# Optimization experiments

Hardware: AMD Instinct MI355X
Metric: run time of the kernel (lower is better)

The kernel has to match this reference:

```python
import jax, jax.numpy as jnp
import numpy as np

N_NODES = 100000
N_EDGES = 1600000
IN_DIM = 128
HIDDEN = 128
OUT_DIM = 64


def setup_inputs() -> dict:
    key = jax.random.key(0)
    k_x, k_e, k_w1, k_b1, k_w2, k_b2 = jax.random.split(key, 6)
    x = jax.random.normal(k_x, (N_NODES, IN_DIM), dtype=jnp.float32)
    edge_index = jax.random.randint(k_e, (2, N_EDGES), 0, N_NODES, dtype=jnp.int64)
    # GCNConv weight/bias (glorot-ish scale) and final Linear head
    W1 = jax.random.normal(k_w1, (IN_DIM, HIDDEN), dtype=jnp.float32) / np.sqrt(IN_DIM)
    b1 = jnp.zeros((HIDDEN,), dtype=jnp.float32)
    W2 = jax.random.normal(k_w2, (HIDDEN, OUT_DIM), dtype=jnp.float32) / np.sqrt(HIDDEN)
    b2 = jnp.zeros((OUT_DIM,), dtype=jnp.float32)
    return {"x": x, "W1": W1, "b1": b1, "W2": W2, "b2": b2, "edge_index": edge_index}


def _gcn_conv(x, W, b, src, dst, norm, n_nodes):
    # PyG GCNConv: linear transform, then sym-normalized neighbor aggregation
    h = x @ W                                   # (N, H) dense transform
    msg = h[src] * norm[:, None]                # (E+N, H) gather + scale
    out = jax.ops.segment_sum(msg, dst, num_segments=n_nodes)  # scatter-add
    return out + b


def reference(x, W1, b1, W2, b2, edge_index):
    n = x.shape[0]
    # add self-loops (PyG GCNConv default)
    loop = jnp.arange(n, dtype=edge_index.dtype)
    src = jnp.concatenate([edge_index[0], loop])
    dst = jnp.concatenate([edge_index[1], loop])
    # symmetric normalization D^{-1/2} A D^{-1/2}
    deg = jnp.zeros((n,), dtype=x.dtype).at[dst].add(1.0)
    dinv = jnp.where(deg > 0, jax.lax.rsqrt(jnp.maximum(deg, 1.0)), 0.0)
    norm = dinv[src] * dinv[dst]

    h = _gcn_conv(x, W1, b1, src, dst, norm, n)
    h = jax.nn.relu(h)
    # dropout: identity in eval/inference mode
    return h @ W2 + b2
```

## Files before the change

kernel.cpp:

```cpp
#include <hip/hip_runtime.h>

#define N_NODES 100000
#define N_EDGES 1600000
#define IN_DIM  128
#define HIDDEN  128
#define OUT_DIM 64

#define BUCK_SHIFT 6
#define BUCK_SZ    64
#define NB_BUCK ((N_NODES + BUCK_SZ - 1) / BUCK_SZ)
#define EPB 4096
#define NBLK_E ((N_EDGES + EPB - 1) / EPB)
#define GB1 ((N_NODES + 127) / 128)
#define CAP 1536
#define PCAP 1984

typedef __attribute__((ext_vector_type(8))) short bf8_t;
typedef __attribute__((ext_vector_type(4))) float f4_t;

__device__ __forceinline__ ushort f2b(float f) {
    unsigned int u = __float_as_uint(f);
    u += 0x7fffu + ((u >> 16) & 1u);
    return (ushort)(u >> 16);
}
__device__ __forceinline__ float b2f_lo(unsigned int u) { return __uint_as_float(u << 16); }
__device__ __forceinline__ float b2f_hi(unsigned int u) { return __uint_as_float(u & 0xffff0000u); }


__global__ __launch_bounds__(256, 2) void k_fuse1(const int* __restrict__ ei,
                                                  int* __restrict__ cursor,
                                                  unsigned int* __restrict__ part,
                                                  const float* __restrict__ x,
                                                  const float* __restrict__ W1,
                                                  ushort* __restrict__ h) {
    __shared__ __align__(16) ushort smem[2 * 128 * 136];
    int tid = threadIdx.x;

    if (blockIdx.x < NBLK_E) {
        int* lh    = (int*)smem;
        int* lbase = lh + NB_BUCK;
        for (int i = tid; i < NB_BUCK; i += 256) lh[i] = 0;
        __syncthreads();
        int e0 = blockIdx.x * EPB;
        int srcv[EPB / 256], dstv[EPB / 256];
        #pragma unroll
        for (int j = 0; j < EPB / 256; j++) {
            int e = e0 + j * 256 + tid;
            if (e < N_EDGES) {
                srcv[j] = ei[e];
                dstv[j] = ei[N_EDGES + e];
                atomicAdd(&lh[dstv[j] >> BUCK_SHIFT], 1);
            } else dstv[j] = -1;
        }
        __syncthreads();
        for (int i = tid; i < NB_BUCK; i += 256) {
            int c = lh[i];
            lbase[i] = (c > 0) ? (i * CAP + atomicAdd(&cursor[i], c)) : 0;
            lh[i] = 0;
        }
        __syncthreads();
        #pragma unroll
        for (int j = 0; j < EPB / 256; j++) {
            if (dstv[j] >= 0) {
                int b = dstv[j] >> BUCK_SHIFT;
                int pos = lbase[b] + atomicAdd(&lh[b], 1);
                part[pos] = ((unsigned int)(dstv[j] & (BUCK_SZ - 1)) << 24) | (unsigned int)srcv[j];
            }
        }
        return;
    }

    typedef ushort (*tile_t)[136];
    tile_t As = (tile_t)smem;
    tile_t Bs = (tile_t)(smem + 128 * 136);
    int row0 = (blockIdx.x - NBLK_E) * 128;
    const int M = N_NODES;

    #pragma unroll
    for (int i = 0; i < 16; i++) {
        int li = tid + i * 256;
        int r = li >> 5, c4 = li & 31;
        int grow = row0 + r; if (grow > M - 1) grow = M - 1;
        float4 v = *(const float4*)(x + (size_t)grow * 128 + c4 * 4);
        ushort4 o;
        o.x = f2b(v.x); o.y = f2b(v.y); o.z = f2b(v.z); o.w = f2b(v.w);
        *(ushort4*)&As[r][c4 * 4] = o;
    }
    #pragma unroll
    for (int i = 0; i < 16; i++) {
        int li = tid + i * 256;
        int k = li >> 5, n4 = li & 31;
        float4 v = *(const float4*)(W1 + (size_t)k * 128 + n4 * 4);
        Bs[n4 * 4 + 0][k] = f2b(v.x);
        Bs[n4 * 4 + 1][k] = f2b(v.y);
        Bs[n4 * 4 + 2][k] = f2b(v.z);
        Bs[n4 * 4 + 3][k] = f2b(v.w);
    }
    __syncthreads();

    int wave = tid >> 6, lane = tid & 63;
    int lr = lane & 15, lq = lane >> 4;
    int wm0 = (wave & 1) * 64;
    int wn0 = (wave >> 1) * 64;

    f4_t acc[4][4];
    #pragma unroll
    for (int mi = 0; mi < 4; mi++)
        #pragma unroll
        for (int ni = 0; ni < 4; ni++) acc[mi][ni] = (f4_t){0.f, 0.f, 0.f, 0.f};

    #pragma unroll
    for (int kb = 0; kb < 4; kb++) {
        bf8_t af[4], bfr[4];
        #pragma unroll
        for (int mi = 0; mi < 4; mi++)
            af[mi] = *(const bf8_t*)&As[wm0 + mi * 16 + lr][kb * 32 + lq * 8];
        #pragma unroll
        for (int ni = 0; ni < 4; ni++)
            bfr[ni] = *(const bf8_t*)&Bs[wn0 + ni * 16 + lr][kb * 32 + lq * 8];
        #pragma unroll
        for (int mi = 0; mi < 4; mi++)
            #pragma unroll
            for (int ni = 0; ni < 4; ni++)
                acc[mi][ni] = __builtin_amdgcn_mfma_f32_16x16x32_bf16(
                    af[mi], bfr[ni], acc[mi][ni], 0, 0, 0);
    }

    #pragma unroll
    for (int mi = 0; mi < 4; mi++) {
        #pragma unroll
        for (int r = 0; r < 4; r++) {
            int row = row0 + wm0 + mi * 16 + lq * 4 + r;
            if (row < M) {
                #pragma unroll
                for (int ni = 0; ni < 4; ni++)
                    h[(size_t)row * 128 + wn0 + ni * 16 + lr] = f2b(acc[mi][ni][r]);
            }
        }
    }
}


__global__ __launch_bounds__(256) void k_csr(const unsigned int* __restrict__ part,
                                             const int* __restrict__ cursor,
                                             int* __restrict__ offs,
                                             int* __restrict__ pcnt,
                                             float* __restrict__ dinv,
                                             int* __restrict__ ssrc,
                                             ushort* __restrict__ h) {
    __shared__ int ldeg[BUCK_SZ], lsc[BUCK_SZ], lcur[BUCK_SZ], sob[BUCK_SZ];
    __shared__ unsigned int stage[CAP];
    int t = threadIdx.x;
    int b = blockIdx.x;
    int rbeg = b * CAP;
    int cnt = cursor[b];
    int node0 = b << BUCK_SHIFT;
    if (b == 0) {
        if (t == 0) dinv[N_NODES] = 0.f;
        if (t < 128) h[(size_t)N_NODES * 128 + t] = 0;
    }
    if (t < BUCK_SZ) ldeg[t] = 0;
    __syncthreads();
    for (int i = t; i < cnt; i += 256) {
        unsigned int u = part[rbeg + i];
        stage[i] = u;
        atomicAdd(&ldeg[u >> 24], 1);
    }
    __syncthreads();
    int v = 0, pv = 0;
    if (t < BUCK_SZ) {
        v = ldeg[t];
        pv = (v + 7) & ~7;
        lsc[t] = pv;
    }
    __syncthreads();
    for (int off = 1; off < BUCK_SZ; off <<= 1) {
        int add = 0;
        if (t < BUCK_SZ && t >= off) add = lsc[t - off];
        __syncthreads();
        if (t < BUCK_SZ) lsc[t] += add;
        __syncthreads();
    }
    if (t < BUCK_SZ) {
        int ob = b * PCAP + (lsc[t] - pv);
        sob[t] = ob;
        lcur[t] = 0;
        if (node0 + t < N_NODES) {
            offs[node0 + t] = ob;
            pcnt[node0 + t] = pv;
            dinv[node0 + t] = rsqrtf((float)(v + 1));
        }
    }
    __syncthreads();
    for (int i = t; i < cnt; i += 256) {
        unsigned int u = stage[i];
        int d = u >> 24;
        int pos = atomicAdd(&lcur[d], 1);
        ssrc[sob[d] + pos] = (int)(u & 0xFFFFFFu);
    }
    if (t < BUCK_SZ)
        for (int i = v; i < pv; i++) ssrc[sob[t] + i] = N_NODES;
}


__global__ __launch_bounds__(256, 7) void k_agg2(const ushort* __restrict__ h,
                                                 const int* __restrict__ offs,
                                                 const int* __restrict__ pcnt,
                                                 const int* __restrict__ ssrc,
                                                 const float* __restrict__ dinv,
                                                 const float* __restrict__ b1,
                                                 const float* __restrict__ W2,
                                                 const float* __restrict__ b2,
                                                 float* __restrict__ out) {
    __shared__ ushort As[16][136];
    __shared__ ushort Bs[64][136];
    int tid = threadIdx.x;
    int wave = tid >> 6, lane = tid & 63;
    int base = blockIdx.x * 16;

    #pragma unroll
    for (int i = 0; i < 8; i++) {
        int li = tid + i * 256;
        int k = li >> 4, n4 = li & 15;
        float4 v = *(const float4*)(W2 + (size_t)k * 64 + n4 * 4);
        Bs[n4 * 4 + 0][k] = f2b(v.x);
        Bs[n4 * 4 + 1][k] = f2b(v.y);
        Bs[n4 * 4 + 2][k] = f2b(v.z);
        Bs[n4 * 4 + 3][k] = f2b(v.w);
    }

    const unsigned int* hp = (const unsigned int*)h;
    float2 bb = ((const float2*)b1)[lane];

    #pragma unroll 1
    for (int j = 0; j < 4; j++) {
        int r = wave * 4 + j;
        int n = base + r;
        int e0 = __builtin_amdgcn_readfirstlane(offs[n]);
        int iters = __builtin_amdgcn_readfirstlane(pcnt[n]) >> 3;
        const uint4* ip = (const uint4*)(ssrc + e0);

        float ax0 = 0.f, ay0 = 0.f, ax1 = 0.f, ay1 = 0.f;
        float ax2 = 0.f, ay2 = 0.f, ax3 = 0.f, ay3 = 0.f;
        uint4 i0, i1;
        if (iters > 0) { i0 = ip[0]; i1 = ip[1]; }
        for (int it = 0; it < iters; it++) {
            uint4 nx0 = i0, nx1 = i1;
            if (it + 1 < iters) { nx0 = ip[(it + 1) * 2]; nx1 = ip[(it + 1) * 2 + 1]; }
            int s0 = __builtin_amdgcn_readfirstlane((int)i0.x);
            int s1 = __builtin_amdgcn_readfirstlane((int)i0.y);
            int s2 = __builtin_amdgcn_readfirstlane((int)i0.z);
            int s3 = __builtin_amdgcn_readfirstlane((int)i0.w);
            int s4 = __builtin_amdgcn_readfirstlane((int)i1.x);
            int s5 = __builtin_amdgcn_readfirstlane((int)i1.y);
            int s6 = __builtin_amdgcn_readfirstlane((int)i1.z);
            int s7 = __builtin_amdgcn_readfirstlane((int)i1.w);
            unsigned int u0 = (hp + ((unsigned)s0 << 6))[lane];
            unsigned int u1 = (hp + ((unsigned)s1 << 6))[lane];
            unsigned int u2 = (hp + ((unsigned)s2 << 6))[lane];
            unsigned int u3 = (hp + ((unsigned)s3 << 6))[lane];
            unsigned int u4 = (hp + ((unsigned)s4 << 6))[lane];
            unsigned int u5 = (hp + ((unsigned)s5 << 6))[lane];
            unsigned int u6 = (hp + ((unsigned)s6 << 6))[lane];
            unsigned int u7 = (hp + ((unsigned)s7 << 6))[lane];
            float w0 = dinv[s0], w1 = dinv[s1], w2 = dinv[s2], w3 = dinv[s3];
            float w4 = dinv[s4], w5 = dinv[s5], w6 = dinv[s6], w7 = dinv[s7];
            ax0 = fmaf(b2f_lo(u0), w0, ax0); ay0 = fmaf(b2f_hi(u0), w0, ay0);
            ax1 = fmaf(b2f_lo(u1), w1, ax1); ay1 = fmaf(b2f_hi(u1), w1, ay1);
            ax2 = fmaf(b2f_lo(u2), w2, ax2); ay2 = fmaf(b2f_hi(u2), w2, ay2);
            ax3 = fmaf(b2f_lo(u3), w3, ax3); ay3 = fmaf(b2f_hi(u3), w3, ay3);
            ax0 = fmaf(b2f_lo(u4), w4, ax0); ay0 = fmaf(b2f_hi(u4), w4, ay0);
            ax1 = fmaf(b2f_lo(u5), w5, ax1); ay1 = fmaf(b2f_hi(u5), w5, ay1);
            ax2 = fmaf(b2f_lo(u6), w6, ax2); ay2 = fmaf(b2f_hi(u6), w6, ay2);
            ax3 = fmaf(b2f_lo(u7), w7, ax3); ay3 = fmaf(b2f_hi(u7), w7, ay3);
            i0 = nx0; i1 = nx1;
        }
        unsigned int us = hp[(size_t)n * 64 + lane];
        float dn = dinv[n];
        float rx = (ax0 + ax1 + ax2 + ax3 + b2f_lo(us) * dn) * dn + bb.x;
        float ry = (ay0 + ay1 + ay2 + ay3 + b2f_hi(us) * dn) * dn + bb.y;
        rx = rx > 0.f ? rx : 0.f;
        ry = ry > 0.f ? ry : 0.f;
        *(unsigned int*)&As[r][lane * 2] =
            ((unsigned int)f2b(ry) << 16) | (unsigned int)f2b(rx);
    }
    __syncthreads();

    int lr = lane & 15, lq = lane >> 4;
    f4_t acc = (f4_t){0.f, 0.f, 0.f, 0.f};
    #pragma unroll
    for (int kb = 0; kb < 4; kb++) {
        bf8_t af = *(const bf8_t*)&As[lr][kb * 32 + lq * 8];
        bf8_t bf = *(const bf8_t*)&Bs[wave * 16 + lr][kb * 32 + lq * 8];
        acc = __builtin_amdgcn_mfma_f32_16x16x32_bf16(af, bf, acc, 0, 0, 0);
    }
    int col = wave * 16 + lr;
    float bv = b2[col];
    #pragma unroll
    for (int r = 0; r < 4; r++) {
        int node = base + lq * 4 + r;
        out[(size_t)node * 64 + col] = acc[r] + bv;
    }
}


extern "C" void kernel_launch(void* const* d_in, const int* in_sizes, int n_in,
                              void* d_out, int out_size, void* d_ws, size_t ws_size,
                              hipStream_t stream) {
    const float* x  = (const float*)d_in[0];
    const float* W1 = (const float*)d_in[1];
    const float* b1 = (const float*)d_in[2];
    const float* W2 = (const float*)d_in[3];
    const float* b2 = (const float*)d_in[4];
    const int*   ei = (const int*)d_in[5];
    float* out = (float*)d_out;

    char* w = (char*)d_ws;
    size_t off = 0;
    auto alloc = [&](size_t bytes) -> void* {
        void* p = w + off;
        off += (bytes + 255) & ~(size_t)255;
        return p;
    };
    ushort* h      = (ushort*)alloc((size_t)(N_NODES + 1) * HIDDEN * 2);
    float* dinv    = (float*)alloc((size_t)(N_NODES + 1) * 4);
    int*   offs    = (int*)alloc((size_t)N_NODES * 4);
    int*   pcnt    = (int*)alloc((size_t)N_NODES * 4);
    int*   ssrc    = (int*)alloc((size_t)NB_BUCK * PCAP * 4);
    unsigned int* part = (unsigned int*)alloc((size_t)NB_BUCK * CAP * 4);
    int*   cursor  = (int*)alloc((size_t)NB_BUCK * 4);

    hipMemsetAsync(cursor, 0, (size_t)NB_BUCK * 4, stream);
    k_fuse1<<<NBLK_E + GB1, 256, 0, stream>>>(ei, cursor, part, x, W1, h);
    k_csr<<<NB_BUCK, 256, 0, stream>>>(part, cursor, offs, pcnt, dinv, ssrc, h);
    k_agg2<<<N_NODES / 16, 256, 0, stream>>>(h, offs, pcnt, ssrc, dinv, b1, W2, b2, out);
}
```

Measured before the change: 217.5 us.

## Split edge bucketing into count, scan, and scatter kernels; pre-convert W1 once

Replaces the single-pass bucketing, which used global atomics on per-bucket cursors, with three kernels. The first counts edges per block and bucket, the second runs a per-bucket prefix scan over blocks, and the third writes edges deterministically using only shared-memory atomics. W1 is converted to bf16 in transposed layout once by a small prep kernel, and the GEMM blocks read it straight from global memory instead of each staging it in LDS. This halves LDS use so occupancy can rise. The cost is three extra launches, edge_index being read twice, and a serial scan of about 391 steps per bucket.

```diff
diff --git a/kernel.cpp b/kernel.cpp
--- a/kernel.cpp
+++ b/kernel.cpp
@@ -14,6 +14,7 @@
 #define GB1 ((N_NODES + 127) / 128)
 #define CAP 1536
 #define PCAP 1984
+#define CSTRIDE 1600
 
 typedef __attribute__((ext_vector_type(8))) short bf8_t;
 typedef __attribute__((ext_vector_type(4))) float f4_t;
@@ -26,53 +27,43 @@
 __device__ __forceinline__ float b2f_lo(unsigned int u) { return __uint_as_float(u << 16); }
 __device__ __forceinline__ float b2f_hi(unsigned int u) { return __uint_as_float(u & 0xffff0000u); }
 
-
-__global__ __launch_bounds__(256, 2) void k_fuse1(const int* __restrict__ ei,
-                                                  int* __restrict__ cursor,
-                                                  unsigned int* __restrict__ part,
-                                                  const float* __restrict__ x,
-                                                  const float* __restrict__ W1,
-                                                  ushort* __restrict__ h) {
-    __shared__ __align__(16) ushort smem[2 * 128 * 136];
+__global__ __launch_bounds__(256) void k_prep(const float* __restrict__ W1,
+                                              ushort* __restrict__ w1b) {
+    int start = blockIdx.x * 2048;
+    #pragma unroll
+    for (int j = 0; j < 8; j++) {
+        int i = start + j * 256 + threadIdx.x;
+        int n = i >> 7, k = i & 127;
+        w1b[i] = f2b(W1[k * 128 + n]);
+    }
+}
+
+__global__ __launch_bounds__(256, 3) void k_cnt(const int* __restrict__ ei,
+                                                int* __restrict__ counts,
+                                                const float* __restrict__ x,
+                                                const ushort* __restrict__ w1b,
+                                                ushort* __restrict__ h) {
+    __shared__ __align__(16) ushort smem[128 * 136];
     int tid = threadIdx.x;
 
     if (blockIdx.x < NBLK_E) {
-        int* lh    = (int*)smem;
-        int* lbase = lh + NB_BUCK;
+        int* lh = (int*)smem;
         for (int i = tid; i < NB_BUCK; i += 256) lh[i] = 0;
         __syncthreads();
         int e0 = blockIdx.x * EPB;
-        int srcv[EPB / 256], dstv[EPB / 256];
         #pragma unroll
         for (int j = 0; j < EPB / 256; j++) {
             int e = e0 + j * 256 + tid;
-            if (e < N_EDGES) {
-                srcv[j] = ei[e];
-                dstv[j] = ei[N_EDGES + e];
-                atomicAdd(&lh[dstv[j] >> BUCK_SHIFT], 1);
-            } else dstv[j] = -1;
+            if (e < N_EDGES) atomicAdd(&lh[ei[N_EDGES + e] >> BUCK_SHIFT], 1);
         }
         __syncthreads();
-        for (int i = tid; i < NB_BUCK; i += 256) {
-            int c = lh[i];
-            lbase[i] = (c > 0) ? (i * CAP + atomicAdd(&cursor[i], c)) : 0;
-            lh[i] = 0;
-        }
-        __syncthreads();
-        #pragma unroll
-        for (int j = 0; j < EPB / 256; j++) {
-            if (dstv[j] >= 0) {
-                int b = dstv[j] >> BUCK_SHIFT;
-                int pos = lbase[b] + atomicAdd(&lh[b], 1);
-                part[pos] = ((unsigned int)(dstv[j] & (BUCK_SZ - 1)) << 24) | (unsigned int)srcv[j];
-            }
-        }
+        for (int i = tid; i < NB_BUCK; i += 256)
+            counts[(size_t)blockIdx.x * CSTRIDE + i] = lh[i];
         return;
     }
 
     typedef ushort (*tile_t)[136];
     tile_t As = (tile_t)smem;
-    tile_t Bs = (tile_t)(smem + 128 * 136);
     int row0 = (blockIdx.x - NBLK_E) * 128;
     const int M = N_NODES;
 
@@ -86,16 +77,6 @@
         o.x = f2b(v.x); o.y = f2b(v.y); o.z = f2b(v.z); o.w = f2b(v.w);
         *(ushort4*)&As[r][c4 * 4] = o;
     }
-    #pragma unroll
-    for (int i = 0; i < 16; i++) {
-        int li = tid + i * 256;
-        int k = li >> 5, n4 = li & 31;
-        float4 v = *(const float4*)(W1 + (size_t)k * 128 + n4 * 4);
-        Bs[n4 * 4 + 0][k] = f2b(v.x);
-        Bs[n4 * 4 + 1][k] = f2b(v.y);
-        Bs[n4 * 4 + 2][k] = f2b(v.z);
-        Bs[n4 * 4 + 3][k] = f2b(v.w);
-    }
     __syncthreads();
 
     int wave = tid >> 6, lane = tid & 63;
@@ -117,7 +98,7 @@
             af[mi] = *(const bf8_t*)&As[wm0 + mi * 16 + lr][kb * 32 + lq * 8];
         #pragma unroll
         for (int ni = 0; ni < 4; ni++)
-            bfr[ni] = *(const bf8_t*)&Bs[wn0 + ni * 16 + lr][kb * 32 + lq * 8];
+            bfr[ni] = *(const bf8_t*)(w1b + (size_t)(wn0 + ni * 16 + lr) * 128 + kb * 32 + lq * 8);
         #pragma unroll
         for (int mi = 0; mi < 4; mi++)
             #pragma unroll
@@ -140,6 +121,41 @@
     }
 }
 
+__global__ __launch_bounds__(256) void k_scan(int* __restrict__ counts,
+                                              int* __restrict__ cursor) {
+    int b = blockIdx.x * 256 + threadIdx.x;
+    if (b >= NB_BUCK) return;
+    int run = b * CAP;
+    #pragma unroll 8
+    for (int blk = 0; blk < NBLK_E; blk++) {
+        size_t idx = (size_t)blk * CSTRIDE + b;
+        int c = counts[idx];
+        counts[idx] = run;
+        run += c;
+    }
+    cursor[b] = run - b * CAP;
+}
+
+__global__ __launch_bounds__(256, 8) void k_part(const int* __restrict__ ei,
+                                                 const int* __restrict__ counts,
+                                                 unsigned int* __restrict__ part) {
+    __shared__ int lcur[NB_BUCK];
+    int tid = threadIdx.x, blk = blockIdx.x;
+    for (int i = tid; i < NB_BUCK; i += 256)
+        lcur[i] = counts[(size_t)blk * CSTRIDE + i];
+    __syncthreads();
+    int e0 = blk * EPB;
+    #pragma unroll
+    for (int j = 0; j < EPB / 256; j++) {
+        int e = e0 + j * 256 + tid;
+        if (e < N_EDGES) {
+            int src = ei[e], dst = ei[N_EDGES + e];
+            int b = dst >> BUCK_SHIFT;
+            int pos = atomicAdd(&lcur[b], 1);
+            part[pos] = ((unsigned int)(dst & (BUCK_SZ - 1)) << 24) | (unsigned int)src;
+        }
+    }
+}
 
 __global__ __launch_bounds__(256) void k_csr(const unsigned int* __restrict__ part,
                                              const int* __restrict__ cursor,
@@ -201,7 +217,6 @@
     if (t < BUCK_SZ)
         for (int i = v; i < pv; i++) ssrc[sob[t] + i] = N_NODES;
 }
-
 
 __global__ __launch_bounds__(256, 7) void k_agg2(const ushort* __restrict__ h,
                                                  const int* __restrict__ offs,
@@ -329,9 +344,13 @@
     int*   ssrc    = (int*)alloc((size_t)NB_BUCK * PCAP * 4);
     unsigned int* part = (unsigned int*)alloc((size_t)NB_BUCK * CAP * 4);
     int*   cursor  = (int*)alloc((size_t)NB_BUCK * 4);
-
-    hipMemsetAsync(cursor, 0, (size_t)NB_BUCK * 4, stream);
-    k_fuse1<<<NBLK_E + GB1, 256, 0, stream>>>(ei, cursor, part, x, W1, h);
+    int*   counts  = (int*)alloc((size_t)NBLK_E * CSTRIDE * 4);
+    ushort* w1b    = (ushort*)alloc((size_t)HIDDEN * IN_DIM * 2);
+
+    k_prep<<<8, 256, 0, stream>>>(W1, w1b);
+    k_cnt<<<NBLK_E + GB1, 256, 0, stream>>>(ei, counts, x, w1b, h);
+    k_scan<<<(NB_BUCK + 255) / 256, 256, 0, stream>>>(counts, cursor);
+    k_part<<<NBLK_E, 256, 0, stream>>>(ei, counts, part);
     k_csr<<<NB_BUCK, 256, 0, stream>>>(part, cursor, offs, pcnt, dinv, ssrc, h);
     k_agg2<<<N_NODES / 16, 256, 0, stream>>>(h, offs, pcnt, ssrc, dinv, b1, W2, b2, out);
 }
```

Measured after the change: 262.1 us. 1.21x slower.

## Replace bucketed CSR build with per-node degree count and direct atomic scatter

Applied to the files above, without the earlier changes.

Replaces the two-pass bucket partition and staging kernel with a global per-node degree histogram, a wave-level scan kernel that computes padded offsets and dinv, and a scatter kernel that places each source directly using per-node atomic cursors. W1 is converted to transposed bf16 once in a small pre-kernel, and the GEMM reads it from global memory instead of building a shared B tile per block, halving shared memory. This removes the part buffer and the intermediate bucket pass. In exchange the edge list is read twice, global atomics on random node addresses are more contended and scattered, and there is one more kernel launch.

```diff
diff --git a/kernel.cpp b/kernel.cpp
--- a/kernel.cpp
+++ b/kernel.cpp
@@ -12,7 +12,6 @@
 #define EPB 4096
 #define NBLK_E ((N_EDGES + EPB - 1) / EPB)
 #define GB1 ((N_NODES + 127) / 128)
-#define CAP 1536
 #define PCAP 1984
 
 typedef __attribute__((ext_vector_type(8))) short bf8_t;
@@ -26,45 +25,83 @@
 __device__ __forceinline__ float b2f_lo(unsigned int u) { return __uint_as_float(u << 16); }
 __device__ __forceinline__ float b2f_hi(unsigned int u) { return __uint_as_float(u & 0xffff0000u); }
 
-
-__global__ __launch_bounds__(256, 2) void k_fuse1(const int* __restrict__ ei,
-                                                  int* __restrict__ cursor,
-                                                  unsigned int* __restrict__ part,
-                                                  const float* __restrict__ x,
-                                                  const float* __restrict__ W1,
-                                                  ushort* __restrict__ h) {
-    __shared__ __align__(16) ushort smem[2 * 128 * 136];
+__global__ __launch_bounds__(256) void k_cp(const int* __restrict__ ei,
+                                            int* __restrict__ deg,
+                                            const float* __restrict__ W1,
+                                            ushort* __restrict__ w1b,
+                                            float* __restrict__ dinv,
+                                            ushort* __restrict__ h) {
     int tid = threadIdx.x;
+    int b = blockIdx.x;
+    if (b < NBLK_E) {
+        int e0 = b * EPB;
+        #pragma unroll
+        for (int j = 0; j < EPB / 256; j++) {
+            int e = e0 + j * 256 + tid;
+            if (e < N_EDGES) atomicAdd(&deg[ei[N_EDGES + e]], 1);
+        }
+        return;
+    }
+    int start = (b - NBLK_E) * 2048;
+    #pragma unroll
+    for (int j = 0; j < 8; j++) {
+        int i = start + j * 256 + tid;
+        int n = i >> 7, k = i & 127;
+        w1b[i] = f2b(W1[k * 128 + n]);
+    }
+    if (b == NBLK_E) {
+        if (tid == 0) dinv[N_NODES] = 0.f;
+        if (tid < 128) h[(size_t)N_NODES * 128 + tid] = 0;
+    }
+}
+
+__global__ __launch_bounds__(256) void k_off(const int* __restrict__ deg,
+                                             int* __restrict__ offs,
+                                             int* __restrict__ pcnt,
+                                             int* __restrict__ ncur,
+                                             float* __restrict__ dinv,
+                                             int* __restrict__ ssrc) {
+    int wave = threadIdx.x >> 6, lane = threadIdx.x & 63;
+    int b = blockIdx.x * 4 + wave;
+    if (b >= NB_BUCK) return;
+    int n = (b << BUCK_SHIFT) + lane;
+    int v = (n < N_NODES) ? deg[n] : 0;
+    int pv = (v + 7) & ~7;
+    int sc = pv;
+    #pragma unroll
+    for (int off = 1; off < 64; off <<= 1) {
+        int u = __shfl_up(sc, off, 64);
+        if (lane >= off) sc += u;
+    }
+    int ob = b * PCAP + (sc - pv);
+    if (n < N_NODES) {
+        offs[n] = ob;
+        pcnt[n] = pv;
+        ncur[n] = 0;
+        dinv[n] = rsqrtf((float)(v + 1));
+        for (int i = v; i < pv; i++) ssrc[ob + i] = N_NODES;
+    }
+}
+
+__global__ __launch_bounds__(256, 3) void k_sg(const int* __restrict__ ei,
+                                               const int* __restrict__ offs,
+                                               int* __restrict__ ncur,
+                                               int* __restrict__ ssrc,
+                                               const float* __restrict__ x,
+                                               const ushort* __restrict__ w1b,
+                                               ushort* __restrict__ h) {
+    __shared__ __align__(16) ushort smem[128 * 136];
+    int tid = threadIdx.x;
 
     if (blockIdx.x < NBLK_E) {
-        int* lh    = (int*)smem;
-        int* lbase = lh + NB_BUCK;
-        for (int i = tid; i < NB_BUCK; i += 256) lh[i] = 0;
-        __syncthreads();
         int e0 = blockIdx.x * EPB;
-        int srcv[EPB / 256], dstv[EPB / 256];
         #pragma unroll
         for (int j = 0; j < EPB / 256; j++) {
             int e = e0 + j * 256 + tid;
             if (e < N_EDGES) {
-                srcv[j] = ei[e];
-                dstv[j] = ei[N_EDGES + e];
-                atomicAdd(&lh[dstv[j] >> BUCK_SHIFT], 1);
-            } else dstv[j] = -1;
-        }
-        __syncthreads();
-        for (int i = tid; i < NB_BUCK; i += 256) {
-            int c = lh[i];
-            lbase[i] = (c > 0) ? (i * CAP + atomicAdd(&cursor[i], c)) : 0;
-            lh[i] = 0;
-        }
-        __syncthreads();
-        #pragma unroll
-        for (int j = 0; j < EPB / 256; j++) {
-            if (dstv[j] >= 0) {
-                int b = dstv[j] >> BUCK_SHIFT;
-                int pos = lbase[b] + atomicAdd(&lh[b], 1);
-                part[pos] = ((unsigned int)(dstv[j] & (BUCK_SZ - 1)) << 24) | (unsigned int)srcv[j];
+                int src = ei[e], dst = ei[N_EDGES + e];
+                int pos = atomicAdd(&ncur[dst], 1);
+                ssrc[offs[dst] + pos] = src;
             }
         }
         return;
@@ -72,7 +109,6 @@
 
     typedef ushort (*tile_t)[136];
     tile_t As = (tile_t)smem;
-    tile_t Bs = (tile_t)(smem + 128 * 136);
     int row0 = (blockIdx.x - NBLK_E) * 128;
     const int M = N_NODES;
 
@@ -86,16 +122,6 @@
         o.x = f2b(v.x); o.y = f2b(v.y); o.z = f2b(v.z); o.w = f2b(v.w);
         *(ushort4*)&As[r][c4 * 4] = o;
     }
-    #pragma unroll
-    for (int i = 0; i < 16; i++) {
-        int li = tid + i * 256;
-        int k = li >> 5, n4 = li & 31;
-        float4 v = *(const float4*)(W1 + (size_t)k * 128 + n4 * 4);
-        Bs[n4 * 4 + 0][k] = f2b(v.x);
-        Bs[n4 * 4 + 1][k] = f2b(v.y);
-        Bs[n4 * 4 + 2][k] = f2b(v.z);
-        Bs[n4 * 4 + 3][k] = f2b(v.w);
-    }
     __syncthreads();
 
     int wave = tid >> 6, lane = tid & 63;
@@ -117,7 +143,7 @@
             af[mi] = *(const bf8_t*)&As[wm0 + mi * 16 + lr][kb * 32 + lq * 8];
         #pragma unroll
         for (int ni = 0; ni < 4; ni++)
-            bfr[ni] = *(const bf8_t*)&Bs[wn0 + ni * 16 + lr][kb * 32 + lq * 8];
+            bfr[ni] = *(const bf8_t*)(w1b + (size_t)(wn0 + ni * 16 + lr) * 128 + kb * 32 + lq * 8);
         #pragma unroll
         for (int mi = 0; mi < 4; mi++)
             #pragma unroll
@@ -139,69 +165,6 @@
         }
     }
 }
-
-
-__global__ __launch_bounds__(256) void k_csr(const unsigned int* __restrict__ part,
-                                             const int* __restrict__ cursor,
-                                             int* __restrict__ offs,
-                                             int* __restrict__ pcnt,
-                                             float* __restrict__ dinv,
-                                             int* __restrict__ ssrc,
-                                             ushort* __restrict__ h) {
-    __shared__ int ldeg[BUCK_SZ], lsc[BUCK_SZ], lcur[BUCK_SZ], sob[BUCK_SZ];
-    __shared__ unsigned int stage[CAP];
-    int t = threadIdx.x;
-    int b = blockIdx.x;
-    int rbeg = b * CAP;
-    int cnt = cursor[b];
-    int node0 = b << BUCK_SHIFT;
-    if (b == 0) {
-        if (t == 0) dinv[N_NODES] = 0.f;
-        if (t < 128) h[(size_t)N_NODES * 128 + t] = 0;
-    }
-    if (t < BUCK_SZ) ldeg[t] = 0;
-    __syncthreads();
-    for (int i = t; i < cnt; i += 256) {
-        unsigned int u = part[rbeg + i];
-        stage[i] = u;
-        atomicAdd(&ldeg[u >> 24], 1);
-    }
-    __syncthreads();
-    int v = 0, pv = 0;
-    if (t < BUCK_SZ) {
-        v = ldeg[t];
-        pv = (v + 7) & ~7;
-        lsc[t] = pv;
-    }
-    __syncthreads();
-    for (int off = 1; off < BUCK_SZ; off <<= 1) {
-        int add = 0;
-        if (t < BUCK_SZ && t >= off) add = lsc[t - off];
-        __syncthreads();
-        if (t < BUCK_SZ) lsc[t] += add;
-        __syncthreads();
-    }
-    if (t < BUCK_SZ) {
-        int ob = b * PCAP + (lsc[t] - pv);
-        sob[t] = ob;
-        lcur[t] = 0;
-        if (node0 + t < N_NODES) {
-            offs[node0 + t] = ob;
-            pcnt[node0 + t] = pv;
-            dinv[node0 + t] = rsqrtf((float)(v + 1));
-        }
-    }
-    __syncthreads();
-    for (int i = t; i < cnt; i += 256) {
-        unsigned int u = stage[i];
-        int d = u >> 24;
-        int pos = atomicAdd(&lcur[d], 1);
-        ssrc[sob[d] + pos] = (int)(u & 0xFFFFFFu);
-    }
-    if (t < BUCK_SZ)
-        for (int i = v; i < pv; i++) ssrc[sob[t] + i] = N_NODES;
-}
-
 
 __global__ __launch_bounds__(256, 7) void k_agg2(const ushort* __restrict__ h,
                                                  const int* __restrict__ offs,
@@ -326,12 +289,14 @@
     float* dinv    = (float*)alloc((size_t)(N_NODES + 1) * 4);
     int*   offs    = (int*)alloc((size_t)N_NODES * 4);
     int*   pcnt    = (int*)alloc((size_t)N_NODES * 4);
+    int*   ncur    = (int*)alloc((size_t)N_NODES * 4);
+    int*   deg     = (int*)alloc((size_t)N_NODES * 4);
     int*   ssrc    = (int*)alloc((size_t)NB_BUCK * PCAP * 4);
-    unsigned int* part = (unsigned int*)alloc((size_t)NB_BUCK * CAP * 4);
-    int*   cursor  = (int*)alloc((size_t)NB_BUCK * 4);
-
-    hipMemsetAsync(cursor, 0, (size_t)NB_BUCK * 4, stream);
-    k_fuse1<<<NBLK_E + GB1, 256, 0, stream>>>(ei, cursor, part, x, W1, h);
-    k_csr<<<NB_BUCK, 256, 0, stream>>>(part, cursor, offs, pcnt, dinv, ssrc, h);
+    ushort* w1b    = (ushort*)alloc((size_t)HIDDEN * IN_DIM * 2);
+
+    hipMemsetAsync(deg, 0, (size_t)N_NODES * 4, stream);
+    k_cp<<<NBLK_E + 8, 256, 0, stream>>>(ei, deg, W1, w1b, dinv, h);
+    k_off<<<(NB_BUCK + 3) / 4, 256, 0, stream>>>(deg, offs, pcnt, ncur, dinv, ssrc);
+    k_sg<<<NBLK_E + GB1, 256, 0, stream>>>(ei, offs, ncur, ssrc, x, w1b, h);
     k_agg2<<<N_NODES / 16, 256, 0, stream>>>(h, offs, pcnt, ssrc, dinv, b1, W2, b2, out);
 }
```

New measurement: 323.3 us. 1.49x slower.

## Pre-convert weights to bf16 once and read MFMA B operands from global

Applied to the files above, without the earlier changes.

Adds a small prep kernel that transposes W1 and W2 to bf16 once. The GEMM and aggregation kernels then load their B fragments straight from global or L2 instead of re-staging the weights into shared memory in every block. This halves shared memory in k_fuse1 and removes Bs from k_agg2, and the occupancy hints are raised to match. Edge binning now uses 16384 edges per block and re-reads the edge indices in the second pass instead of holding them in registers. The cost is one extra launch, repeated global loads of the B fragments, and a second read of the edge list.

```diff
diff --git a/kernel.cpp b/kernel.cpp
--- a/kernel.cpp
+++ b/kernel.cpp
@@ -9,7 +9,7 @@
 #define BUCK_SHIFT 6
 #define BUCK_SZ    64
 #define NB_BUCK ((N_NODES + BUCK_SZ - 1) / BUCK_SZ)
-#define EPB 4096
+#define EPB 16384
 #define NBLK_E ((N_EDGES + EPB - 1) / EPB)
 #define GB1 ((N_NODES + 127) / 128)
 #define CAP 1536
@@ -26,14 +26,43 @@
 __device__ __forceinline__ float b2f_lo(unsigned int u) { return __uint_as_float(u << 16); }
 __device__ __forceinline__ float b2f_hi(unsigned int u) { return __uint_as_float(u & 0xffff0000u); }
 
-
-__global__ __launch_bounds__(256, 2) void k_fuse1(const int* __restrict__ ei,
+__global__ __launch_bounds__(256) void k_prep(const float* __restrict__ W1,
+                                              const float* __restrict__ W2,
+                                              ushort* __restrict__ w1b,
+                                              ushort* __restrict__ w2b,
+                                              float* __restrict__ dinv,
+                                              ushort* __restrict__ h) {
+    int b = blockIdx.x, t = threadIdx.x;
+    if (b < 8) {
+        int start = b * 2048;
+        #pragma unroll
+        for (int j = 0; j < 8; j++) {
+            int i = start + j * 256 + t;
+            int n = i >> 7, k = i & 127;
+            w1b[i] = f2b(W1[k * 128 + n]);
+        }
+        if (b == 0) {
+            if (t == 0) dinv[N_NODES] = 0.f;
+            if (t < 128) h[(size_t)N_NODES * 128 + t] = 0;
+        }
+    } else {
+        int start = (b - 8) * 2048;
+        #pragma unroll
+        for (int j = 0; j < 8; j++) {
+            int i = start + j * 256 + t;
+            int n = i >> 7, k = i & 127;
+            w2b[i] = f2b(W2[k * 64 + n]);
+        }
+    }
+}
+
+__global__ __launch_bounds__(256, 3) void k_fuse1(const int* __restrict__ ei,
                                                   int* __restrict__ cursor,
                                                   unsigned int* __restrict__ part,
                                                   const float* __restrict__ x,
-                                                  const float* __restrict__ W1,
+                                                  const ushort* __restrict__ w1b,
                                                   ushort* __restrict__ h) {
-    __shared__ __align__(16) ushort smem[2 * 128 * 136];
+    __shared__ __align__(16) ushort smem[128 * 136];
     int tid = threadIdx.x;
 
     if (blockIdx.x < NBLK_E) {
@@ -42,15 +71,10 @@
         for (int i = tid; i < NB_BUCK; i += 256) lh[i] = 0;
         __syncthreads();
         int e0 = blockIdx.x * EPB;
-        int srcv[EPB / 256], dstv[EPB / 256];
-        #pragma unroll
+        #pragma unroll 4
         for (int j = 0; j < EPB / 256; j++) {
             int e = e0 + j * 256 + tid;
-            if (e < N_EDGES) {
-                srcv[j] = ei[e];
-                dstv[j] = ei[N_EDGES + e];
-                atomicAdd(&lh[dstv[j] >> BUCK_SHIFT], 1);
-            } else dstv[j] = -1;
+            if (e < N_EDGES) atomicAdd(&lh[ei[N_EDGES + e] >> BUCK_SHIFT], 1);
         }
         __syncthreads();
         for (int i = tid; i < NB_BUCK; i += 256) {
@@ -59,12 +83,14 @@
             lh[i] = 0;
         }
         __syncthreads();
-        #pragma unroll
+        #pragma unroll 4
         for (int j = 0; j < EPB / 256; j++) {
-            if (dstv[j] >= 0) {
-                int b = dstv[j] >> BUCK_SHIFT;
-                int pos = lbase[b] + atomicAdd(&lh[b], 1);
-                part[pos] = ((unsigned int)(dstv[j] & (BUCK_SZ - 1)) << 24) | (unsigned int)srcv[j];
+            int e = e0 + j * 256 + tid;
+            if (e < N_EDGES) {
+                int src = ei[e], dst = ei[N_EDGES + e];
+                int bk = dst >> BUCK_SHIFT;
+                int pos = lbase[bk] + atomicAdd(&lh[bk], 1);
+                part[pos] = ((unsigned int)(dst & (BUCK_SZ - 1)) << 24) | (unsigned int)src;
             }
         }
         return;
@@ -72,7 +98,6 @@
 
     typedef ushort (*tile_t)[136];
     tile_t As = (tile_t)smem;
-    tile_t Bs = (tile_t)(smem + 128 * 136);
     int row0 = (blockIdx.x - NBLK_E) * 128;
     const int M = N_NODES;
 
@@ -86,16 +111,6 @@
         o.x = f2b(v.x); o.y = f2b(v.y); o.z = f2b(v.z); o.w = f2b(v.w);
         *(ushort4*)&As[r][c4 * 4] = o;
     }
-    #pragma unroll
-    for (int i = 0; i < 16; i++) {
-        int li = tid + i * 256;
-        int k = li >> 5, n4 = li & 31;
-        float4 v = *(const float4*)(W1 + (size_t)k * 128 + n4 * 4);
-        Bs[n4 * 4 + 0][k] = f2b(v.x);
-        Bs[n4 * 4 + 1][k] = f2b(v.y);
-        Bs[n4 * 4 + 2][k] = f2b(v.z);
-        Bs[n4 * 4 + 3][k] = f2b(v.w);
-    }
     __syncthreads();
 
     int wave = tid >> 6, lane = tid & 63;
@@ -117,7 +132,7 @@
             af[mi] = *(const bf8_t*)&As[wm0 + mi * 16 + lr][kb * 32 + lq * 8];
         #pragma unroll
         for (int ni = 0; ni < 4; ni++)
-            bfr[ni] = *(const bf8_t*)&Bs[wn0 + ni * 16 + lr][kb * 32 + lq * 8];
+            bfr[ni] = *(const bf8_t*)(w1b + (size_t)(wn0 + ni * 16 + lr) * 128 + kb * 32 + lq * 8);
         #pragma unroll
         for (int mi = 0; mi < 4; mi++)
             #pragma unroll
@@ -139,7 +154,6 @@
         }
     }
 }
-
 
 __global__ __launch_bounds__(256) void k_csr(const unsigned int* __restrict__ part,
                                              const int* __restrict__ cursor,
@@ -202,32 +216,19 @@
         for (int i = v; i < pv; i++) ssrc[sob[t] + i] = N_NODES;
 }
 
-
-__global__ __launch_bounds__(256, 7) void k_agg2(const ushort* __restrict__ h,
+__global__ __launch_bounds__(256, 8) void k_agg2(const ushort* __restrict__ h,
                                                  const int* __restrict__ offs,
                                                  const int* __restrict__ pcnt,
                                                  const int* __restrict__ ssrc,
                                                  const float* __restrict__ dinv,
                                                  const float* __restrict__ b1,
-                                                 const float* __restrict__ W2,
+                                                 const ushort* __restrict__ w2b,
                                                  const float* __restrict__ b2,
                                                  float* __restrict__ out) {
     __shared__ ushort As[16][136];
-    __shared__ ushort Bs[64][136];
     int tid = threadIdx.x;
     int wave = tid >> 6, lane = tid & 63;
     int base = blockIdx.x * 16;
-
-    #pragma unroll
-    for (int i = 0; i < 8; i++) {
-        int li = tid + i * 256;
-        int k = li >> 4, n4 = li & 15;
-        float4 v = *(const float4*)(W2 + (size_t)k * 64 + n4 * 4);
-        Bs[n4 * 4 + 0][k] = f2b(v.x);
-        Bs[n4 * 4 + 1][k] = f2b(v.y);
-        Bs[n4 * 4 + 2][k] = f2b(v.z);
-        Bs[n4 * 4 + 3][k] = f2b(v.w);
-    }
 
     const unsigned int* hp = (const unsigned int*)h;
     float2 bb = ((const float2*)b1)[lane];
@@ -291,7 +292,7 @@
     #pragma unroll
     for (int kb = 0; kb < 4; kb++) {
         bf8_t af = *(const bf8_t*)&As[lr][kb * 32 + lq * 8];
-        bf8_t bf = *(const bf8_t*)&Bs[wave * 16 + lr][kb * 32 + lq * 8];
+        bf8_t bf = *(const bf8_t*)(w2b + (size_t)(wave * 16 + lr) * 128 + kb * 32 + lq * 8);
         acc = __builtin_amdgcn_mfma_f32_16x16x32_bf16(af, bf, acc, 0, 0, 0);
     }
     int col = wave * 16 + lr;
@@ -329,9 +330,12 @@
     int*   ssrc    = (int*)alloc((size_t)NB_BUCK * PCAP * 4);
     unsigned int* part = (unsigned int*)alloc((size_t)NB_BUCK * CAP * 4);
     int*   cursor  = (int*)alloc((size_t)NB_BUCK * 4);
+    ushort* w1b    = (ushort*)alloc((size_t)HIDDEN * IN_DIM * 2);
+    ushort* w2b    = (ushort*)alloc((size_t)OUT_DIM * HIDDEN * 2);
 
     hipMemsetAsync(cursor, 0, (size_t)NB_BUCK * 4, stream);
-    k_fuse1<<<NBLK_E + GB1, 256, 0, stream>>>(ei, cursor, part, x, W1, h);
+    k_prep<<<12, 256, 0, stream>>>(W1, W2, w1b, w2b, dinv, h);
+    k_fuse1<<<NBLK_E + GB1, 256, 0, stream>>>(ei, cursor, part, x, w1b, h);
     k_csr<<<NB_BUCK, 256, 0, stream>>>(part, cursor, offs, pcnt, dinv, ssrc, h);
-    k_agg2<<<N_NODES / 16, 256, 0, stream>>>(h, offs, pcnt, ssrc, dinv, b1, W2, b2, out);
-}
+    k_agg2<<<N_NODES / 16, 256, 0, stream>>>(h, offs, pcnt, ssrc, dinv, b1, w2b, b2, out);
+}
```

Result: slower. 249.5 us (+14.7%).
